# Kernel optimization log

Measured on AMD Instinct MI355X. Metric: run time of the kernel, lower is better.

Reference implementation:

```python
import jax, jax.numpy as jnp
import numpy as np

HEADS = 8
DIM_HEAD = 32  # dim // heads


def setup_inputs() -> dict:
    key = jax.random.key(0)
    ks = jax.random.split(key, 5)
    B, C, H, W = 4, 256, 48, 48
    return {
        "x": jax.random.normal(ks[0], (B, C, H, W), jnp.float32),
        "Wqkv": jax.random.normal(ks[1], (3 * C, C), jnp.float32) * (C ** -0.5),
        "bqkv": jax.random.normal(ks[2], (3 * C,), jnp.float32) * 0.02,
        "W0": jax.random.normal(ks[3], (C, C), jnp.float32) * (C ** -0.5),
        "b0": jax.random.normal(ks[4], (C,), jnp.float32) * 0.02,
    }


def reference(x, Wqkv, bqkv, W0, b0):
    b, c, h, w = x.shape
    m, d = HEADS, DIM_HEAD
    n = h * w
    scale = d ** -0.5
    # 1x1 conv == per-pixel GEMM: [b,3c,h,w]
    qkv = jnp.einsum('bchw,oc->bohw', x, Wqkv) + bqkv[None, :, None, None]
    # rearrange 'b (d k m) h w -> k b m (h w) d' (channel factors as d, then k, then m)
    qkv = qkv.reshape(b, d, 3, m, n)            # [b, d, 3, m, n]
    qkv = jnp.transpose(qkv, (2, 0, 3, 4, 1))   # [3, b, m, n, d]
    q, k, v = qkv[0], qkv[1], qkv[2]
    scores = jnp.einsum('bmid,bmjd->bmij', q, k) * scale  # [b, m, n, n]
    attn = jax.nn.softmax(scores, axis=-1)
    out = jnp.einsum('bmij,bmjd->bmid', attn, v)          # [b, m, n, d]
    # rearrange 'b m (h w) d -> b (m d) h w'
    out = jnp.transpose(out, (0, 1, 3, 2)).reshape(b, m * d, h, w)
    out = jnp.einsum('bchw,oc->bohw', out, W0) + b0[None, :, None, None]
    return out
```

## Files before the change

kernel.cpp:

```cpp
#include <hip/hip_runtime.h>
#include <hip/hip_bf16.h>

#define NPIX 2304
#define C_IN 256
#define NHEADS 8
#define DHEAD 32

typedef float f32x4 __attribute__((ext_vector_type(4)));
typedef __bf16 bf16x8 __attribute__((ext_vector_type(8)));
typedef __bf16 bf16x4 __attribute__((ext_vector_type(4)));

#if __has_builtin(__builtin_amdgcn_exp2f)
#define EXP2F(x) __builtin_amdgcn_exp2f(x)
#else
#define EXP2F(x) exp2f(x)
#endif

__device__ inline void gload_lds16(const void* g, void* l) {
    __builtin_amdgcn_global_load_lds(
        (const __attribute__((address_space(1))) unsigned int*)g,
        (__attribute__((address_space(3))) unsigned int*)l, 16, 0, 0);
}

__global__ __launch_bounds__(256) void prep_wx(
    const float* __restrict__ Wq, const float* __restrict__ W0,
    const float* __restrict__ x,
    __bf16* __restrict__ wq, __bf16* __restrict__ w0,
    __bf16* __restrict__ xt)
{
    __shared__ unsigned int lds[64 * 69];
    const int id = blockIdx.x;
    const int t  = threadIdx.x;

    if (id >= 576) {
        const int r = id - 576;
        float v;
        __bf16* dst;
        if (r < 768) { v = Wq[r * 256 + t];         dst = wq + (size_t)r * 512; }
        else         { v = W0[(r - 768) * 256 + t]; dst = w0 + (size_t)(r - 768) * 512; }
        __bf16 hb = (__bf16)v;
        dst[t]       = hb;
        dst[256 + t] = (__bf16)(v - (float)hb);
        return;
    }

    const int n0 = (id % 36) * 64;
    const int c0 = ((id / 36) & 3) * 64;
    const int b  = id / 144;
    const float* xb = x + (size_t)b * C_IN * NPIX;

    #pragma unroll
    for (int p = 0; p < 4; ++p) {
        const int r    = (t >> 4) + p * 16;
        const int ncol = (t & 15) * 4;
        float4 v = *(const float4*)&xb[(size_t)(c0 + r) * NPIX + n0 + ncol];
        float a[4] = {v.x, v.y, v.z, v.w};
        #pragma unroll
        for (int i = 0; i < 4; ++i)
            lds[r * 69 + ncol + i] =
                (unsigned int)__builtin_bit_cast(unsigned short, (__bf16)a[i]);
    }
    __syncthreads();

    #pragma unroll
    for (int p = 0; p < 2; ++p) {
        const int nn = (t >> 3) + p * 32;
        const int ch = t & 7;
        bf16x8 h8;
        #pragma unroll
        for (int i = 0; i < 8; ++i)
            h8[i] = __builtin_bit_cast(__bf16,
                        (unsigned short)lds[(ch * 8 + i) * 69 + nn]);
        *(bf16x8*)&xt[((size_t)b * NPIX + n0 + nn) * 256 + c0 + ch * 8] = h8;
    }
}

__global__ __launch_bounds__(256) void qkv_mfma(
    const __bf16* __restrict__ wq, const __bf16* __restrict__ xt,
    const float* __restrict__ bias, float* __restrict__ qg,
    __bf16* __restrict__ khi, __bf16* __restrict__ vg)
{
    __shared__ alignas(16) unsigned char sm[49152];
    const int tid = threadIdx.x;
    const int l   = tid & 63;
    const int w   = tid >> 6;
    const int g   = l >> 4;
    const int c16 = l & 15;

    const int id  = blockIdx.x;
    const int xcd = id & 7;
    const int li  = id >> 3;
    const int pnl = xcd * 9 + li / 6;
    const int mt  = li % 6;
    const int b   = pnl / 18;
    const int nt  = pnl - b * 18;
    const int n0  = nt * 128;
    const int p0  = mt * 128;
    const int kq  = mt >> 1;

    const int wr = (w >> 1) * 64;
    const int wc = (w & 1) * 64;
    f32x4 acc[4][4] = {};

#define STG(buf, cs)                                                           \
    {                                                                          \
        unsigned char* lbs = sm + (buf) * 24576;                               \
        _Pragma("unroll")                                                      \
        for (int i = 0; i < 4; ++i) {                                          \
            const int row = i * 64 + (tid >> 2);                               \
            const int cl  = tid & 3;                                           \
            const int cg  = cl ^ (row & 3);                                    \
            const int pr  = p0 + (row & 127);                                  \
            const int oA  = 24 * ((pr & 255) >> 3) + 8 * kq + (pr & 7);        \
            gload_lds16(wq + (size_t)oA * 512 + (i >> 1) * 256 +               \
                            (cs) * 32 + cg * 8,                                \
                        lbs + row * 64 + cl * 16);                             \
        }                                                                      \
        _Pragma("unroll")                                                      \
        for (int i = 0; i < 2; ++i) {                                          \
            const int row = i * 64 + (tid >> 2);                               \
            const int cl  = tid & 3;                                           \
            const int cg  = cl ^ (row & 3);                                    \
            gload_lds16(xt + ((size_t)b * NPIX + n0 + row) * 256 +             \
                            (cs) * 32 + cg * 8,                                \
                        lbs + 16384 + row * 64 + cl * 16);                     \
        }                                                                      \
    }

    STG(0, 0);
    __syncthreads();
    #pragma unroll
    for (int cs = 0; cs < 8; ++cs) {
        const int buf = cs & 1;
        if (cs + 1 < 8) STG(buf ^ 1, cs + 1);
        unsigned char* lb = sm + buf * 24576;
        bf16x8 ah[4], al4[4], bf4[4];
        #pragma unroll
        for (int oi = 0; oi < 4; ++oi) {
            const int ra = wr + oi * 16 + c16;
            ah[oi]  = *(bf16x8*)(lb + ra * 64 + ((g ^ (ra & 3)) * 16));
            al4[oi] = *(bf16x8*)(lb + (128 + ra) * 64 + ((g ^ (ra & 3)) * 16));
        }
        #pragma unroll
        for (int ni = 0; ni < 4; ++ni) {
            const int rb = wc + ni * 16 + c16;
            bf4[ni] = *(bf16x8*)(lb + 16384 + rb * 64 + ((g ^ (rb & 3)) * 16));
        }
        #pragma unroll
        for (int oi = 0; oi < 4; ++oi)
            #pragma unroll
            for (int ni = 0; ni < 4; ++ni) {
                acc[oi][ni] = __builtin_amdgcn_mfma_f32_16x16x32_bf16(
                    ah[oi], bf4[ni], acc[oi][ni], 0, 0, 0);
                acc[oi][ni] = __builtin_amdgcn_mfma_f32_16x16x32_bf16(
                    al4[oi], bf4[ni], acc[oi][ni], 0, 0, 0);
            }
        __syncthreads();
    }
#undef STG

    const float qscale = 0.17677669529663687f * 1.4426950408889634f;
    #pragma unroll
    for (int oi = 0; oi < 4; ++oi) {
        #pragma unroll
        for (int rr = 0; rr < 4; ++rr) {
            const int p = p0 + wr + oi * 16 + 4 * g + rr;
            const int d = (p & 255) >> 3;
            const int h = p & 7;
            const int o = 24 * d + 8 * kq + h;
            const float bi = bias[o];
            const int bh_ = b * NHEADS + h;
            #pragma unroll
            for (int ni = 0; ni < 4; ++ni) {
                const int n = n0 + wc + ni * 16 + c16;
                const float val = acc[oi][ni][rr] + bi;
                if (kq == 0) {
                    qg[((size_t)bh_ * DHEAD + d) * NPIX + n] = val * qscale;
                } else if (kq == 1) {
                    const int cp = ((d >> 3) + (n >> 1)) & 3;
                    khi[((size_t)bh_ * NPIX + n) * 32 + cp * 8 + (d & 7)] = (__bf16)val;
                } else {
                    const int cp = ((n >> 3) & 7) ^ (d & 7);
                    vg[((size_t)bh_ * DHEAD + d) * NPIX + (n >> 6) * 64 + cp * 8 + (n & 7)]
                        = (__bf16)val;
                }
            }
        }
    }
}

__global__ __launch_bounds__(256) void attn_mfma(
    const float* __restrict__ qg, const __bf16* __restrict__ khi,
    const __bf16* __restrict__ vg,
    float* __restrict__ po, float* __restrict__ lw)
{
    __shared__ alignas(16) unsigned char sm[32768];
    const int tid = threadIdx.x;
    const int l   = tid & 63;
    const int w   = tid >> 6;
    const int g   = l >> 4;
    const int c16 = l & 15;

    const int id = blockIdx.x;
    const int lg = (id & 7) * 144 + (id >> 3);
    const int bh = lg / 36;
    const int rem = lg - bh * 36;
    const int half = rem / 18;
    const int qt = rem - half * 18;

    const float*  qb  = qg  + (size_t)bh * DHEAD * NPIX;
    const __bf16* khb = khi + (size_t)bh * NPIX * 32;
    const __bf16* vb  = vg  + (size_t)bh * DHEAD * NPIX;

    const int q0 = qt * 128 + w * 32;

    bf16x8 qh[2], ql[2];
    #pragma unroll
    for (int qgi = 0; qgi < 2; ++qgi)
        #pragma unroll
        for (int e = 0; e < 8; ++e) {
            float v = qb[(size_t)(g * 8 + e) * NPIX + q0 + qgi * 16 + c16];
            __bf16 hb = (__bf16)v;
            qh[qgi][e] = hb;
            ql[qgi][e] = (__bf16)(v - (float)hb);
        }

    f32x4 o[2][2] = {};
    float lsum[2] = {0.f, 0.f};

    const int vd   = w * 8 + (l >> 3);
    const int kswz = (c16 >> 1) & 3;
    unsigned char* const wsl = sm + 16384 + w * 4096;

#define STAGE(buf, kb)                                                         \
    {                                                                          \
        const int j0s = (kb) * 64;                                             \
        unsigned char* lbs = sm + (buf) * 8192;                                \
        gload_lds16(khb + (size_t)(j0s + w * 16) * 32 + l * 8, lbs + w * 1024);\
        gload_lds16(vb + (size_t)vd * NPIX + j0s + (l & 7) * 8,                \
                    lbs + 4096 + w * 1024);                                    \
    }

    const int kb0 = half * 18;
    STAGE(0, kb0);
    __syncthreads();

    for (int t = 0; t < 18; ++t) {
        const int buf = t & 1;
        if (t + 1 < 18) STAGE(buf ^ 1, kb0 + t + 1);
        unsigned char* lb = sm + buf * 8192;

        f32x4 sv[2][4];
        __builtin_amdgcn_s_setprio(1);
        #pragma unroll
        for (int f = 0; f < 4; ++f) {
            const int ko = (c16 + 16 * f) * 64 + ((g + kswz) & 3) * 16;
            bf16x8 kh8 = *(bf16x8*)(lb + ko);
            #pragma unroll
            for (int qgi = 0; qgi < 2; ++qgi) {
                f32x4 acc = {0.f, 0.f, 0.f, 0.f};
                acc = __builtin_amdgcn_mfma_f32_16x16x32_bf16(kh8, ql[qgi], acc, 0, 0, 0);
                acc = __builtin_amdgcn_mfma_f32_16x16x32_bf16(kh8, qh[qgi], acc, 0, 0, 0);
                sv[qgi][f] = acc;
            }
        }
        __builtin_amdgcn_s_setprio(0);

        #pragma unroll
        for (int qgi = 0; qgi < 2; ++qgi) {
            float rs = 0.f;
            __bf16 pb[16];
            #pragma unroll
            for (int f = 0; f < 4; ++f)
                #pragma unroll
                for (int rr = 0; rr < 4; ++rr) {
                    const float p = EXP2F(sv[qgi][f][rr]);
                    rs += p;
                    pb[f * 4 + rr] = (__bf16)p;
                }
            lsum[qgi] += rs;
            const int qrow = qgi * 16 + c16;
            #pragma unroll
            for (int f = 0; f < 4; ++f) {
                const int ch = (2 * f + (g >> 1)) ^ (c16 & 7);
                *(bf16x4*)(wsl + qrow * 128 + ch * 16 + (g & 1) * 8) =
                    *(bf16x4*)&pb[f * 4];
            }
        }

        __builtin_amdgcn_s_setprio(1);
        #pragma unroll
        for (int kc = 0; kc < 2; ++kc) {
            const int vch = (((g + 4 * kc) ^ (c16 & 7))) * 16;
            bf16x8 va0 = *(bf16x8*)(lb + 4096 + c16 * 128 + vch);
            bf16x8 va1 = *(bf16x8*)(lb + 4096 + (16 + c16) * 128 + vch);
            #pragma unroll
            for (int qgi = 0; qgi < 2; ++qgi) {
                bf16x8 pf = *(bf16x8*)(wsl + (qgi * 16 + c16) * 128 + vch);
                o[qgi][0] = __builtin_amdgcn_mfma_f32_16x16x32_bf16(va0, pf, o[qgi][0], 0, 0, 0);
                o[qgi][1] = __builtin_amdgcn_mfma_f32_16x16x32_bf16(va1, pf, o[qgi][1], 0, 0, 0);
            }
        }
        __builtin_amdgcn_s_setprio(0);

        __syncthreads();
    }
#undef STAGE

    #pragma unroll
    for (int qgi = 0; qgi < 2; ++qgi) {
        lsum[qgi] += __shfl_xor(lsum[qgi], 16);
        lsum[qgi] += __shfl_xor(lsum[qgi], 32);
        const int n = q0 + qgi * 16 + c16;
        const size_t rbase = ((size_t)(half * 32 + bh) * NPIX + n) * 32;
        #pragma unroll
        for (int dh = 0; dh < 2; ++dh)
            *(f32x4*)&po[rbase + dh * 16 + 4 * g] = o[qgi][dh];
        if (g == 0)
            lw[(size_t)(half * 32 + bh) * NPIX + n] = lsum[qgi];
    }
}

__global__ __launch_bounds__(256) void out_mfma(
    const __bf16* __restrict__ w0, const float* __restrict__ po,
    const float* __restrict__ lw, const float* __restrict__ bias,
    float* __restrict__ out)
{
    __shared__ alignas(16) unsigned char sm[51200];
    const int tid = threadIdx.x;
    const int l   = tid & 63;
    const int w   = tid >> 6;
    const int g   = l >> 4;
    const int c16 = l & 15;

    const int id  = blockIdx.x;
    const int xcd = id & 7;
    const int li  = id >> 3;
    const int pnl = xcd * 9 + (li >> 1);
    const int mt  = li & 1;
    const int b   = pnl / 18;
    const int nt  = pnl - b * 18;
    const int n0  = nt * 128;
    const int o0  = mt * 128;

    const int wr = (w >> 1) * 64;
    const int wc = (w & 1) * 64;
    f32x4 acc[4][4] = {};

    const int brow = tid >> 1;
    const int bch  = tid & 1;

#define STG_A(buf, cs)                                                         \
    {                                                                          \
        unsigned char* lbs = sm + (buf) * 25600;                               \
        _Pragma("unroll")                                                      \
        for (int i = 0; i < 4; ++i) {                                          \
            const int row = i * 64 + (tid >> 2);                               \
            const int cl  = tid & 3;                                           \
            const int cg  = cl ^ (row & 3);                                    \
            gload_lds16(w0 + (size_t)(o0 + (row & 127)) * 512 +                \
                            (i >> 1) * 256 + (cs) * 32 + cg * 8,               \
                        lbs + row * 64 + cl * 16);                             \
        }                                                                      \
    }

    f32x4 r0[4], r1[4];
    float il;

#define LDB(cs)                                                                \
    {                                                                          \
        const int bh_ = b * 8 + (cs);                                          \
        const int n   = n0 + brow;                                             \
        const float l0 = lw[(size_t)bh_ * NPIX + n];                           \
        const float l1 = lw[(size_t)(32 + bh_) * NPIX + n];                    \
        il = 1.0f / (l0 + l1);                                                 \
        const float* s0 = &po[((size_t)bh_ * NPIX + n) * 32 + bch * 16];       \
        const float* s1 = &po[((size_t)(32 + bh_) * NPIX + n) * 32 + bch * 16];\
        _Pragma("unroll")                                                      \
        for (int k2 = 0; k2 < 4; ++k2) {                                       \
            r0[k2] = *(const f32x4*)(s0 + k2 * 4);                             \
            r1[k2] = *(const f32x4*)(s1 + k2 * 4);                             \
        }                                                                      \
    }

#define WRB(buf)                                                               \
    {                                                                          \
        unsigned char* lbs = sm + (buf) * 25600 + 16384;                       \
        _Pragma("unroll")                                                      \
        for (int k2 = 0; k2 < 2; ++k2) {                                       \
            bf16x8 v8;                                                         \
            _Pragma("unroll")                                                  \
            for (int e = 0; e < 4; ++e) {                                      \
                v8[e]     = (__bf16)((r0[2 * k2][e]     + r1[2 * k2][e])     * il); \
                v8[4 + e] = (__bf16)((r0[2 * k2 + 1][e] + r1[2 * k2 + 1][e]) * il); \
            }                                                                  \
            *(bf16x8*)(lbs + brow * 72 + bch * 32 + k2 * 16) = v8;             \
        }                                                                      \
    }

    STG_A(0, 0);
    LDB(0);
    WRB(0);
    __syncthreads();

    #pragma unroll
    for (int cs = 0; cs < 8; ++cs) {
        const int buf = cs & 1;
        if (cs + 1 < 8) {
            STG_A(buf ^ 1, cs + 1);
            LDB(cs + 1);
        }
        unsigned char* lb = sm + buf * 25600;
        bf16x8 ah[4], al4[4], bf4[4];
        #pragma unroll
        for (int oi = 0; oi < 4; ++oi) {
            const int ra = wr + oi * 16 + c16;
            ah[oi]  = *(bf16x8*)(lb + ra * 64 + ((g ^ (ra & 3)) * 16));
            al4[oi] = *(bf16x8*)(lb + (128 + ra) * 64 + ((g ^ (ra & 3)) * 16));
        }
        #pragma unroll
        for (int ni = 0; ni < 4; ++ni) {
            const int rb = wc + ni * 16 + c16;
            bf4[ni] = *(bf16x8*)(lb + 16384 + rb * 72 + g * 16);
        }
        #pragma unroll
        for (int oi = 0; oi < 4; ++oi)
            #pragma unroll
            for (int ni = 0; ni < 4; ++ni) {
                acc[oi][ni] = __builtin_amdgcn_mfma_f32_16x16x32_bf16(
                    ah[oi], bf4[ni], acc[oi][ni], 0, 0, 0);
                acc[oi][ni] = __builtin_amdgcn_mfma_f32_16x16x32_bf16(
                    al4[oi], bf4[ni], acc[oi][ni], 0, 0, 0);
            }
        if (cs + 1 < 8) WRB(buf ^ 1);
        __syncthreads();
    }
#undef STG_A
#undef LDB
#undef WRB

    #pragma unroll
    for (int oi = 0; oi < 4; ++oi) {
        #pragma unroll
        for (int rr = 0; rr < 4; ++rr) {
            const int o = o0 + wr + oi * 16 + 4 * g + rr;
            const float bi = bias[o];
            #pragma unroll
            for (int ni = 0; ni < 4; ++ni) {
                const int n = n0 + wc + ni * 16 + c16;
                out[((size_t)b * C_IN + o) * NPIX + n] = acc[oi][ni][rr] + bi;
            }
        }
    }
}

extern "C" void kernel_launch(void* const* d_in, const int* in_sizes, int n_in,
                              void* d_out, int out_size, void* d_ws, size_t ws_size,
                              hipStream_t stream) {
    const float* x    = (const float*)d_in[0];
    const float* Wqkv = (const float*)d_in[1];
    const float* bqkv = (const float*)d_in[2];
    const float* W0   = (const float*)d_in[3];
    const float* b0   = (const float*)d_in[4];
    float* out = (float*)d_out;

    char* ws = (char*)d_ws;
    __bf16* wq  = (__bf16*)(ws);
    __bf16* w0  = (__bf16*)(ws + 786432);
    __bf16* xt  = (__bf16*)(ws + 1048576);
    float*  qg  = (float*) (ws + 5767168);
    __bf16* khi = (__bf16*)(ws + 15204352);
    __bf16* vg  = (__bf16*)(ws + 19922944);
    float*  po  = (float*) (ws + 24641536);
    float*  lw  = (float*) (ws + 43515904);

    prep_wx<<<dim3(1600), 256, 0, stream>>>(Wqkv, W0, x, wq, w0, xt);
    qkv_mfma<<<dim3(432), 256, 0, stream>>>(wq, xt, bqkv, qg, khi, vg);
    attn_mfma<<<dim3(1152), 256, 0, stream>>>(qg, khi, vg, po, lw);
    out_mfma<<<dim3(144), 256, 0, stream>>>(w0, po, lw, b0, out);
}
```

Measured before the change: 156.8 us.

## Store Q as bf16 token-major, drop split-precision QK, halve GEMM tile heights

Q is now written by the QKV GEMM as bf16 in a token-major layout, so the attention kernel loads it with one vector load per fragment. The hi/lo split MFMA for QK^T is dropped, which halves the score MFMAs and shrinks the Q workspace. The QKV and output projection GEMMs switch to 64-row output tiles, doubling their grid sizes and reducing LDS use to raise parallelism and occupancy. The cost is lower accuracy in the attention scores and more redundant B-tile loads across blocks.

Measured after the change: 158.8 us. Within noise of the previous version (+1.2%).

```diff
diff --git a/kernel.cpp b/kernel.cpp
--- a/kernel.cpp
+++ b/kernel.cpp
@@ -77,10 +77,10 @@
 
 __global__ __launch_bounds__(256) void qkv_mfma(
     const __bf16* __restrict__ wq, const __bf16* __restrict__ xt,
-    const float* __restrict__ bias, float* __restrict__ qg,
+    const float* __restrict__ bias, __bf16* __restrict__ qt,
     __bf16* __restrict__ khi, __bf16* __restrict__ vg)
 {
-    __shared__ alignas(16) unsigned char sm[49152];
+    __shared__ alignas(16) unsigned char sm[32768];
     const int tid = threadIdx.x;
     const int l   = tid & 63;
     const int w   = tid >> 6;
@@ -90,30 +90,29 @@
     const int id  = blockIdx.x;
     const int xcd = id & 7;
     const int li  = id >> 3;
-    const int pnl = xcd * 9 + li / 6;
-    const int mt  = li % 6;
+    const int pnl = xcd * 9 + li / 12;
+    const int mtt = li % 12;
     const int b   = pnl / 18;
     const int nt  = pnl - b * 18;
     const int n0  = nt * 128;
-    const int p0  = mt * 128;
-    const int kq  = mt >> 1;
-
-    const int wr = (w >> 1) * 64;
-    const int wc = (w & 1) * 64;
-    f32x4 acc[4][4] = {};
+    const int kq  = mtt >> 2;
+    const int seg = (mtt & 3) * 64;
+
+    const int wo = (w >> 1) * 32;
+    const int wn = (w & 1) * 64;
+    f32x4 acc[2][4] = {};
 
 #define STG(buf, cs)                                                           \
     {                                                                          \
-        unsigned char* lbs = sm + (buf) * 24576;                               \
+        unsigned char* lbs = sm + (buf) * 16384;                               \
         _Pragma("unroll")                                                      \
-        for (int i = 0; i < 4; ++i) {                                          \
+        for (int i = 0; i < 2; ++i) {                                          \
             const int row = i * 64 + (tid >> 2);                               \
             const int cl  = tid & 3;                                           \
             const int cg  = cl ^ (row & 3);                                    \
-            const int pr  = p0 + (row & 127);                                  \
-            const int oA  = 24 * ((pr & 255) >> 3) + 8 * kq + (pr & 7);        \
-            gload_lds16(wq + (size_t)oA * 512 + (i >> 1) * 256 +               \
-                            (cs) * 32 + cg * 8,                                \
+            const int pp  = seg + (row & 63);                                  \
+            const int oA  = 24 * (pp >> 3) + 8 * kq + (pp & 7);                \
+            gload_lds16(wq + (size_t)oA * 512 + i * 256 + (cs) * 32 + cg * 8,  \
                         lbs + row * 64 + cl * 16);                             \
         }                                                                      \
         _Pragma("unroll")                                                      \
@@ -123,7 +122,7 @@
             const int cg  = cl ^ (row & 3);                                    \
             gload_lds16(xt + ((size_t)b * NPIX + n0 + row) * 256 +             \
                             (cs) * 32 + cg * 8,                                \
-                        lbs + 16384 + row * 64 + cl * 16);                     \
+                        lbs + 8192 + row * 64 + cl * 16);                      \
         }                                                                      \
     }
 
@@ -133,27 +132,27 @@
     for (int cs = 0; cs < 8; ++cs) {
         const int buf = cs & 1;
         if (cs + 1 < 8) STG(buf ^ 1, cs + 1);
-        unsigned char* lb = sm + buf * 24576;
-        bf16x8 ah[4], al4[4], bf4[4];
-        #pragma unroll
-        for (int oi = 0; oi < 4; ++oi) {
-            const int ra = wr + oi * 16 + c16;
+        unsigned char* lb = sm + buf * 16384;
+        bf16x8 ah[2], al2[2], bf4[4];
+        #pragma unroll
+        for (int oi = 0; oi < 2; ++oi) {
+            const int ra = wo + oi * 16 + c16;
             ah[oi]  = *(bf16x8*)(lb + ra * 64 + ((g ^ (ra & 3)) * 16));
-            al4[oi] = *(bf16x8*)(lb + (128 + ra) * 64 + ((g ^ (ra & 3)) * 16));
+            al2[oi] = *(bf16x8*)(lb + (64 + ra) * 64 + ((g ^ (ra & 3)) * 16));
         }
         #pragma unroll
         for (int ni = 0; ni < 4; ++ni) {
-            const int rb = wc + ni * 16 + c16;
-            bf4[ni] = *(bf16x8*)(lb + 16384 + rb * 64 + ((g ^ (rb & 3)) * 16));
-        }
-        #pragma unroll
-        for (int oi = 0; oi < 4; ++oi)
+            const int rb = wn + ni * 16 + c16;
+            bf4[ni] = *(bf16x8*)(lb + 8192 + rb * 64 + ((g ^ (rb & 3)) * 16));
+        }
+        #pragma unroll
+        for (int oi = 0; oi < 2; ++oi)
             #pragma unroll
             for (int ni = 0; ni < 4; ++ni) {
                 acc[oi][ni] = __builtin_amdgcn_mfma_f32_16x16x32_bf16(
                     ah[oi], bf4[ni], acc[oi][ni], 0, 0, 0);
                 acc[oi][ni] = __builtin_amdgcn_mfma_f32_16x16x32_bf16(
-                    al4[oi], bf4[ni], acc[oi][ni], 0, 0, 0);
+                    al2[oi], bf4[ni], acc[oi][ni], 0, 0, 0);
             }
         __syncthreads();
     }
@@ -161,21 +160,21 @@
 
     const float qscale = 0.17677669529663687f * 1.4426950408889634f;
     #pragma unroll
-    for (int oi = 0; oi < 4; ++oi) {
+    for (int oi = 0; oi < 2; ++oi) {
         #pragma unroll
         for (int rr = 0; rr < 4; ++rr) {
-            const int p = p0 + wr + oi * 16 + 4 * g + rr;
-            const int d = (p & 255) >> 3;
-            const int h = p & 7;
-            const int o = 24 * d + 8 * kq + h;
+            const int pp = seg + wo + oi * 16 + 4 * g + rr;
+            const int d  = pp >> 3;
+            const int h  = pp & 7;
+            const int o  = 24 * d + 8 * kq + h;
             const float bi = bias[o];
             const int bh_ = b * NHEADS + h;
             #pragma unroll
             for (int ni = 0; ni < 4; ++ni) {
-                const int n = n0 + wc + ni * 16 + c16;
+                const int n = n0 + wn + ni * 16 + c16;
                 const float val = acc[oi][ni][rr] + bi;
                 if (kq == 0) {
-                    qg[((size_t)bh_ * DHEAD + d) * NPIX + n] = val * qscale;
+                    qt[((size_t)bh_ * NPIX + n) * 32 + d] = (__bf16)(val * qscale);
                 } else if (kq == 1) {
                     const int cp = ((d >> 3) + (n >> 1)) & 3;
                     khi[((size_t)bh_ * NPIX + n) * 32 + cp * 8 + (d & 7)] = (__bf16)val;
@@ -190,7 +189,7 @@
 }
 
 __global__ __launch_bounds__(256) void attn_mfma(
-    const float* __restrict__ qg, const __bf16* __restrict__ khi,
+    const __bf16* __restrict__ qt, const __bf16* __restrict__ khi,
     const __bf16* __restrict__ vg,
     float* __restrict__ po, float* __restrict__ lw)
 {
@@ -206,24 +205,18 @@
     const int bh = lg / 36;
     const int rem = lg - bh * 36;
     const int half = rem / 18;
-    const int qt = rem - half * 18;
-
-    const float*  qb  = qg  + (size_t)bh * DHEAD * NPIX;
+    const int qt_i = rem - half * 18;
+
+    const __bf16* qb  = qt  + (size_t)bh * NPIX * 32;
     const __bf16* khb = khi + (size_t)bh * NPIX * 32;
     const __bf16* vb  = vg  + (size_t)bh * DHEAD * NPIX;
 
-    const int q0 = qt * 128 + w * 32;
-
-    bf16x8 qh[2], ql[2];
+    const int q0 = qt_i * 128 + w * 32;
+
+    bf16x8 qh[2];
     #pragma unroll
     for (int qgi = 0; qgi < 2; ++qgi)
-        #pragma unroll
-        for (int e = 0; e < 8; ++e) {
-            float v = qb[(size_t)(g * 8 + e) * NPIX + q0 + qgi * 16 + c16];
-            __bf16 hb = (__bf16)v;
-            qh[qgi][e] = hb;
-            ql[qgi][e] = (__bf16)(v - (float)hb);
-        }
+        qh[qgi] = *(const bf16x8*)&qb[(size_t)(q0 + qgi * 16 + c16) * 32 + g * 8];
 
     f32x4 o[2][2] = {};
     float lsum[2] = {0.f, 0.f};
@@ -259,7 +252,6 @@
             #pragma unroll
             for (int qgi = 0; qgi < 2; ++qgi) {
                 f32x4 acc = {0.f, 0.f, 0.f, 0.f};
-                acc = __builtin_amdgcn_mfma_f32_16x16x32_bf16(kh8, ql[qgi], acc, 0, 0, 0);
                 acc = __builtin_amdgcn_mfma_f32_16x16x32_bf16(kh8, qh[qgi], acc, 0, 0, 0);
                 sv[qgi][f] = acc;
             }
@@ -326,7 +318,7 @@
     const float* __restrict__ lw, const float* __restrict__ bias,
     float* __restrict__ out)
 {
-    __shared__ alignas(16) unsigned char sm[51200];
+    __shared__ alignas(16) unsigned char sm[34816];
     const int tid = threadIdx.x;
     const int l   = tid & 63;
     const int w   = tid >> 6;
@@ -336,30 +328,30 @@
     const int id  = blockIdx.x;
     const int xcd = id & 7;
     const int li  = id >> 3;
-    const int pnl = xcd * 9 + (li >> 1);
-    const int mt  = li & 1;
+    const int pnl = xcd * 9 + (li >> 2);
+    const int mt  = li & 3;
     const int b   = pnl / 18;
     const int nt  = pnl - b * 18;
     const int n0  = nt * 128;
-    const int o0  = mt * 128;
-
-    const int wr = (w >> 1) * 64;
-    const int wc = (w & 1) * 64;
-    f32x4 acc[4][4] = {};
+    const int o0  = mt * 64;
+
+    const int wo = (w >> 1) * 32;
+    const int wn = (w & 1) * 64;
+    f32x4 acc[2][4] = {};
 
     const int brow = tid >> 1;
     const int bch  = tid & 1;
 
 #define STG_A(buf, cs)                                                         \
     {                                                                          \
-        unsigned char* lbs = sm + (buf) * 25600;                               \
+        unsigned char* lbs = sm + (buf) * 17408;                               \
         _Pragma("unroll")                                                      \
-        for (int i = 0; i < 4; ++i) {                                          \
+        for (int i = 0; i < 2; ++i) {                                          \
             const int row = i * 64 + (tid >> 2);                               \
             const int cl  = tid & 3;                                           \
             const int cg  = cl ^ (row & 3);                                    \
-            gload_lds16(w0 + (size_t)(o0 + (row & 127)) * 512 +                \
-                            (i >> 1) * 256 + (cs) * 32 + cg * 8,               \
+            gload_lds16(w0 + (size_t)(o0 + (row & 63)) * 512 + i * 256 +       \
+                            (cs) * 32 + cg * 8,                                \
                         lbs + row * 64 + cl * 16);                             \
         }                                                                      \
     }
@@ -385,7 +377,7 @@
 
 #define WRB(buf)                                                               \
     {                                                                          \
-        unsigned char* lbs = sm + (buf) * 25600 + 16384;                       \
+        unsigned char* lbs = sm + (buf) * 17408 + 8192;                        \
         _Pragma("unroll")                                                      \
         for (int k2 = 0; k2 < 2; ++k2) {                                       \
             bf16x8 v8;                                                         \
@@ -410,27 +402,27 @@
             STG_A(buf ^ 1, cs + 1);
             LDB(cs + 1);
         }
-        unsigned char* lb = sm + buf * 25600;
-        bf16x8 ah[4], al4[4], bf4[4];
-        #pragma unroll
-        for (int oi = 0; oi < 4; ++oi) {
-            const int ra = wr + oi * 16 + c16;
+        unsigned char* lb = sm + buf * 17408;
+        bf16x8 ah[2], al2[2], bf4[4];
+        #pragma unroll
+        for (int oi = 0; oi < 2; ++oi) {
+            const int ra = wo + oi * 16 + c16;
             ah[oi]  = *(bf16x8*)(lb + ra * 64 + ((g ^ (ra & 3)) * 16));
-            al4[oi] = *(bf16x8*)(lb + (128 + ra) * 64 + ((g ^ (ra & 3)) * 16));
+            al2[oi] = *(bf16x8*)(lb + (64 + ra) * 64 + ((g ^ (ra & 3)) * 16));
         }
         #pragma unroll
         for (int ni = 0; ni < 4; ++ni) {
-            const int rb = wc + ni * 16 + c16;
-            bf4[ni] = *(bf16x8*)(lb + 16384 + rb * 72 + g * 16);
-        }
-        #pragma unroll
-        for (int oi = 0; oi < 4; ++oi)
+            const int rb = wn + ni * 16 + c16;
+            bf4[ni] = *(bf16x8*)(lb + 8192 + rb * 72 + g * 16);
+        }
+        #pragma unroll
+        for (int oi = 0; oi < 2; ++oi)
             #pragma unroll
             for (int ni = 0; ni < 4; ++ni) {
                 acc[oi][ni] = __builtin_amdgcn_mfma_f32_16x16x32_bf16(
                     ah[oi], bf4[ni], acc[oi][ni], 0, 0, 0);
                 acc[oi][ni] = __builtin_amdgcn_mfma_f32_16x16x32_bf16(
-                    al4[oi], bf4[ni], acc[oi][ni], 0, 0, 0);
+                    al2[oi], bf4[ni], acc[oi][ni], 0, 0, 0);
             }
         if (cs + 1 < 8) WRB(buf ^ 1);
         __syncthreads();
@@ -440,14 +432,14 @@
 #undef WRB
 
     #pragma unroll
-    for (int oi = 0; oi < 4; ++oi) {
+    for (int oi = 0; oi < 2; ++oi) {
         #pragma unroll
         for (int rr = 0; rr < 4; ++rr) {
-            const int o = o0 + wr + oi * 16 + 4 * g + rr;
+            const int o = o0 + wo + oi * 16 + 4 * g + rr;
             const float bi = bias[o];
             #pragma unroll
             for (int ni = 0; ni < 4; ++ni) {
-                const int n = n0 + wc + ni * 16 + c16;
+                const int n = n0 + wn + ni * 16 + c16;
                 out[((size_t)b * C_IN + o) * NPIX + n] = acc[oi][ni][rr] + bi;
             }
         }
@@ -468,14 +460,14 @@
     __bf16* wq  = (__bf16*)(ws);
     __bf16* w0  = (__bf16*)(ws + 786432);
     __bf16* xt  = (__bf16*)(ws + 1048576);
-    float*  qg  = (float*) (ws + 5767168);
-    __bf16* khi = (__bf16*)(ws + 15204352);
-    __bf16* vg  = (__bf16*)(ws + 19922944);
-    float*  po  = (float*) (ws + 24641536);
-    float*  lw  = (float*) (ws + 43515904);
+    __bf16* qt  = (__bf16*)(ws + 5767168);
+    __bf16* khi = (__bf16*)(ws + 10485760);
+    __bf16* vg  = (__bf16*)(ws + 15204352);
+    float*  po  = (float*) (ws + 19922944);
+    float*  lw  = (float*) (ws + 38797312);
 
     prep_wx<<<dim3(1600), 256, 0, stream>>>(Wqkv, W0, x, wq, w0, xt);
-    qkv_mfma<<<dim3(432), 256, 0, stream>>>(wq, xt, bqkv, qg, khi, vg);
-    attn_mfma<<<dim3(1152), 256, 0, stream>>>(qg, khi, vg, po, lw);
-    out_mfma<<<dim3(144), 256, 0, stream>>>(w0, po, lw, b0, out);
-}
+    qkv_mfma<<<dim3(864), 256, 0, stream>>>(wq, xt, bqkv, qt, khi, vg);
+    attn_mfma<<<dim3(1152), 256, 0, stream>>>(qt, khi, vg, po, lw);
+    out_mfma<<<dim3(288), 256, 0, stream>>>(w0, po, lw, b0, out);
+}
```
